# Optimization experiments

Hardware: AMD Instinct MI355X
Metric: run time of the kernel (lower is better)

## Reference

```python
import jax, jax.numpy as jnp
import numpy as np

N = 100_000      # nodes
E = 1_600_000    # edges
F_IN = 4         # num_features
H = 128          # hidden_channels
C = 5            # num_classes
G = 256          # graphs in batch


def setup_inputs() -> dict:
    key = jax.random.key(0)
    ks = jax.random.split(key, 14)
    x = jax.random.normal(ks[0], (N, F_IN), dtype=jnp.float32)
    edge_index = jax.random.randint(ks[1], (2, E), 0, N, dtype=jnp.int64)
    batch = jnp.sort(jax.random.randint(ks[2], (N,), 0, G, dtype=jnp.int64))
    def lin(k, fan_in, fan_out):
        kw, kb = jax.random.split(k)
        s = 1.0 / np.sqrt(fan_in)
        W = jax.random.uniform(kw, (fan_in, fan_out), jnp.float32, -s, s)
        b = jax.random.uniform(kb, (fan_out,), jnp.float32, -s, s)
        return W, b
    W1, b1 = lin(ks[3], F_IN, H)
    W2, b2 = lin(ks[4], H, H)
    W3, b3 = lin(ks[5], H, H)
    W4, b4 = lin(ks[6], H, H)
    Wl, bl = lin(ks[7], H, C)
    return {"x": x, "edge_index": edge_index, "batch": batch,
            "W1": W1, "b1": b1, "W2": W2, "b2": b2,
            "W3": W3, "b3": b3, "W4": W4, "b4": b4,
            "Wl": Wl, "bl": bl}


def reference(x, edge_index, batch, W1, b1, W2, b2, W3, b3, W4, b4, Wl, bl):
    n = x.shape[0]
    loop = jnp.arange(n, dtype=edge_index.dtype)
    src = jnp.concatenate([edge_index[0], loop])  # [E+N], with self-loops
    dst = jnp.concatenate([edge_index[1], loop])
    # symmetric normalization on A + I (PyG GCNConv default)
    deg = jax.ops.segment_sum(jnp.ones_like(dst, dtype=x.dtype), dst, num_segments=n)
    dinv = deg ** -0.5  # deg >= 1 thanks to self-loops
    coef = dinv[src] * dinv[dst]  # per-edge norm [E+N]

    def conv(h, W, b):
        h = h @ W                               # [N, H]
        msg = h[src] * coef[:, None]            # gather + scale [E+N, H]
        return jax.ops.segment_sum(msg, dst, num_segments=n) + b

    h = jax.nn.relu(conv(x, W1, b1))
    h = jax.nn.relu(conv(h, W2, b2))
    h = jax.nn.relu(conv(h, W3, b3))
    h = jax.nn.relu(conv(h, W4, b4))

    # global_mean_pool over graph ids
    counts = jax.ops.segment_sum(jnp.ones((n,), h.dtype), batch, num_segments=G)
    pooled = jax.ops.segment_sum(h, batch, num_segments=G)
    pooled = pooled / jnp.maximum(counts, 1.0)[:, None]  # [G, H]

    return jax.nn.sigmoid(pooled @ Wl + bl)  # [G, C]
```

## Files before the change

kernel.cpp:

```cpp
#include <hip/hip_runtime.h>
#include <hip/hip_fp8.h>
#include <math.h>

#define N_NODES 100000
#define N_EDGES 1600000
#define F_IN    4
#define HID     128
#define N_CLS   5
#define N_GRAPH 256
#define POOL_SEG 8

#define BSHIFT   9
#define BSIZE    512
#define NBUK     196
#define NCHUNK   200
#define CHUNK    8000

typedef _Float16 f16;
typedef _Float16 f16x2 __attribute__((ext_vector_type(2)));
typedef _Float16 f16x8 __attribute__((ext_vector_type(8)));
typedef float f32x4 __attribute__((ext_vector_type(4)));

__device__ __forceinline__ float rec_coef(unsigned r) {
    return (float)__builtin_bit_cast(_Float16, (unsigned short)(r & 0x7FFFu));
}

__device__ __forceinline__ f16x2 rec_coef2(unsigned r) {
    unsigned c = r & 0x7FFFu;
    return __builtin_bit_cast(f16x2, (c << 16) | c);
}

__device__ __forceinline__ float2 fp8x2_to_f32x2(unsigned short raw) {
    __hip_fp8x2_e4m3 t;
    t.__x = raw;
    return static_cast<float2>(t);
}

#if __has_builtin(__builtin_amdgcn_cvt_pk_f16_fp8)
__device__ __forceinline__ f16x2 cvt_h2(unsigned v) {
    auto t = __builtin_amdgcn_cvt_pk_f16_fp8((short)v);
    return __builtin_bit_cast(f16x2, t);
}
#else
__device__ __forceinline__ f16x2 cvt_h2(unsigned v) {
    float2 f = fp8x2_to_f32x2((unsigned short)v);
    auto t = __builtin_amdgcn_cvt_pkrtz(f.x, f.y);
    return __builtin_bit_cast(f16x2, t);
}
#endif

__device__ __forceinline__ void fma8h(f16x2 c2, uint2 v, f16x2* acc) {
    acc[0] += c2 * cvt_h2(v.x);
    acc[1] += c2 * cvt_h2(v.x >> 16);
    acc[2] += c2 * cvt_h2(v.y);
    acc[3] += c2 * cvt_h2(v.y >> 16);
}

__device__ __forceinline__ f16x2 shfl_xor_h2(f16x2 a, int m) {
    return __builtin_bit_cast(f16x2, __shfl_xor(__builtin_bit_cast(int, a), m, 64));
}

__global__ __launch_bounds__(256) void k_bc(const int* __restrict__ dst, int* __restrict__ C) {
    __shared__ int cnt[NBUK];
    int t = threadIdx.x;
    if (t < NBUK) cnt[t] = 0;
    __syncthreads();
    int base = blockIdx.x * CHUNK;
#pragma unroll
    for (int it = 0; it < 32; ++it) {
        int idx = it * 256 + t;
        if (idx < CHUNK) atomicAdd(&cnt[dst[base + idx] >> BSHIFT], 1);
    }
    __syncthreads();
    if (t < NBUK) C[blockIdx.x * NBUK + t] = cnt[t];
}

__global__ __launch_bounds__(256) void k_bscan(const int* __restrict__ C, int* __restrict__ Off,
                                               int* __restrict__ bbase) {
    __shared__ int s[256];
    int b = threadIdx.x;
    int tot = 0;
    if (b < NBUK) {
        for (int c = 0; c < NCHUNK; ++c) {
            Off[c * NBUK + b] = tot;
            tot += C[c * NBUK + b];
        }
    }
    s[b] = (b < NBUK) ? tot : 0;
    __syncthreads();
    for (int off = 1; off < 256; off <<= 1) {
        int v = (b >= off) ? s[b - off] : 0;
        __syncthreads();
        s[b] += v;
        __syncthreads();
    }
    if (b < NBUK) bbase[b] = s[b] - tot;
    if (b == 0) bbase[NBUK] = N_EDGES;
}

__global__ __launch_bounds__(256) void k_scatter(const int* __restrict__ src, const int* __restrict__ dst,
                                                 const int* __restrict__ Off, const int* __restrict__ bbase,
                                                 unsigned* __restrict__ bkt) {
    __shared__ int cur[NBUK];
    int t = threadIdx.x;
    if (t < NBUK) cur[t] = bbase[t] + Off[blockIdx.x * NBUK + t];
    __syncthreads();
    int base = blockIdx.x * CHUNK;
#pragma unroll
    for (int it = 0; it < 32; ++it) {
        int idx = it * 256 + t;
        if (idx < CHUNK) {
            int s = src[base + idx], d = dst[base + idx];
            int b = d >> BSHIFT;
            int p = atomicAdd(&cur[b], 1);
            bkt[p] = ((unsigned)s << BSHIFT) | (unsigned)(d & (BSIZE - 1));
        }
    }
}

__global__ __launch_bounds__(256) void k_hist2(const unsigned* __restrict__ bkt,
                                               const int* __restrict__ bbase,
                                               int* __restrict__ deg, float* __restrict__ dinv,
                                               int* __restrict__ padTot) {
    __shared__ int hist[BSIZE];
    __shared__ int tot;
    int t = threadIdx.x, b = blockIdx.x;
    hist[t] = 0; hist[t + 256] = 0;
    if (t == 0) tot = 0;
    __syncthreads();
    int s0 = bbase[b], s1 = bbase[b + 1];
    for (int e = s0 + t; e < s1; e += 256) atomicAdd(&hist[bkt[e] & (BSIZE - 1)], 1);
    __syncthreads();
    int loc = 0;
#pragma unroll
    for (int h = 0; h < 2; ++h) {
        int l = t + h * 256;
        int node = b * BSIZE + l;
        int d = hist[l];
        if (node < N_NODES) {
            deg[node] = d;
            dinv[node] = rsqrtf((float)d + 1.0f);
        }
        loc += (d + 15) >> 4;
    }
    atomicAdd(&tot, loc);
    __syncthreads();
    if (t == 0) padTot[b] = tot << 4;
}

__global__ __launch_bounds__(256) void k_pscan(const int* __restrict__ padTot, int* __restrict__ padBase,
                                               int* __restrict__ rowptrP) {
    __shared__ int s[256];
    int b = threadIdx.x;
    int v = (b < NBUK) ? padTot[b] : 0;
    s[b] = v;
    __syncthreads();
    for (int off = 1; off < 256; off <<= 1) {
        int u = (b >= off) ? s[b - off] : 0;
        __syncthreads();
        s[b] += u;
        __syncthreads();
    }
    if (b < NBUK) padBase[b] = s[b] - v;
    if (b == 0) {
        padBase[NBUK] = s[NBUK - 1];
        rowptrP[N_NODES] = s[NBUK - 1];
    }
}

__global__ __launch_bounds__(256) void k_local2(const unsigned* __restrict__ bkt,
                                                const int* __restrict__ bbase,
                                                const int* __restrict__ deg,
                                                const float* __restrict__ dinv,
                                                const int* __restrict__ padBase,
                                                int* __restrict__ rowptrP,
                                                unsigned* __restrict__ edges) {
    __shared__ int sc[BSIZE];
    __shared__ int cur[BSIZE];
    __shared__ int st[BSIZE];
    __shared__ float dv[BSIZE];
    int t = threadIdx.x, b = blockIdx.x;
    int base = padBase[b];
    int n0 = b * BSIZE + t, n1 = n0 + 256;
    int d0 = (n0 < N_NODES) ? deg[n0] : 0;
    int d1 = (n1 < N_NODES) ? deg[n1] : 0;
    int p0 = ((d0 + 15) >> 4) << 4;
    int p1 = ((d1 + 15) >> 4) << 4;
    sc[t] = p0; sc[t + 256] = p1;
    dv[t] = (n0 < N_NODES) ? dinv[n0] : 0.f;
    dv[t + 256] = (n1 < N_NODES) ? dinv[n1] : 0.f;
    __syncthreads();
    for (int off = 1; off < BSIZE; off <<= 1) {
        int i0 = t, i1 = t + 256;
        int v0 = (i0 >= off) ? sc[i0 - off] : 0;
        int v1 = (i1 >= off) ? sc[i1 - off] : 0;
        __syncthreads();
        sc[i0] += v0; sc[i1] += v1;
        __syncthreads();
    }
    int off0 = base + sc[t] - p0;
    int off1 = base + sc[t + 256] - p1;
    if (n0 < N_NODES) rowptrP[n0] = off0;
    if (n1 < N_NODES) rowptrP[n1] = off1;
    cur[t] = off0; cur[t + 256] = off1;
    st[t]  = off0; st[t + 256]  = off1;
    int padT = sc[BSIZE - 1];
    for (int i = base + t; i < base + padT; i += 256) edges[i] = 0;
    __syncthreads();
    int s0 = bbase[b], s1 = bbase[b + 1];
    for (int e = s0 + t; e < s1; e += 256) {
        unsigned r = bkt[e];
        int dl = (int)(r & (BSIZE - 1));
        int s = (int)(r >> BSHIFT);
        int p = atomicAdd(&cur[dl], 1);
        int rs = st[dl];
        int sl = p - rs;
        int phys = rs + (sl & ~15) + (((sl & 3) << 2) | ((sl >> 2) & 3));
        float c = dv[dl] * dinv[s];
        unsigned short cb = __builtin_bit_cast(unsigned short, (f16)c);
        edges[phys] = ((unsigned)s << 15) | (unsigned)(cb & 0x7FFFu);
    }
}

__global__ __launch_bounds__(256) void k_aggx1(const float4* __restrict__ x,
                                               const int* __restrict__ rowptrP,
                                               const unsigned* __restrict__ edges,
                                               const float* __restrict__ dinv,
                                               const float* __restrict__ W1, const float* __restrict__ b1,
                                               unsigned* __restrict__ hA) {
    __shared__ float4 sxa[16];
    __shared__ float sW[4 * HID];
    __shared__ float sb[HID];
    int t = threadIdx.x;
    sW[t] = W1[t];
    sW[t + 256] = W1[t + 256];
    if (t < HID) sb[t] = b1[t];
    int grp = t >> 4;
    int l = t & 15;
    int node = blockIdx.x * 16 + grp;
    int beg = rowptrP[node], end = rowptrP[node + 1];
    float ax = 0.f, ay = 0.f, az = 0.f, aw = 0.f;
    for (int e = beg + l; e < end; e += 16) {
        unsigned r = edges[e];
        float c = rec_coef(r);
        float4 v = x[r >> 15];
        ax = fmaf(c, v.x, ax); ay = fmaf(c, v.y, ay);
        az = fmaf(c, v.z, az); aw = fmaf(c, v.w, aw);
    }
#pragma unroll
    for (int off = 1; off < 16; off <<= 1) {
        ax += __shfl_xor(ax, off, 64);
        ay += __shfl_xor(ay, off, 64);
        az += __shfl_xor(az, off, 64);
        aw += __shfl_xor(aw, off, 64);
    }
    if (l == 0) {
        float di = dinv[node];
        float c0 = di * di;
        float4 xv = x[node];
        sxa[grp] = make_float4(fmaf(c0, xv.x, ax), fmaf(c0, xv.y, ay),
                               fmaf(c0, xv.z, az), fmaf(c0, xv.w, aw));
    }
    __syncthreads();

    int node0 = blockIdx.x * 16;
#pragma unroll
    for (int it = 0; it < 2; ++it) {
        int id = it * 256 + t;
        int n = id >> 5;
        int g = id & 31;
        float4 a = sxa[n];
        float c[4];
#pragma unroll
        for (int j = 0; j < 4; ++j) {
            int col = g * 4 + j;
            float v = sb[col];
            v = fmaf(a.x, sW[col],           v);
            v = fmaf(a.y, sW[HID + col],     v);
            v = fmaf(a.z, sW[2 * HID + col], v);
            v = fmaf(a.w, sW[3 * HID + col], v);
            c[j] = fmaxf(v, 0.0f);
        }
        unsigned lo = __hip_fp8x2_e4m3(make_float2(c[0], c[1])).__x;
        unsigned hi = __hip_fp8x2_e4m3(make_float2(c[2], c[3])).__x;
        hA[(node0 + n) * 32 + g] = lo | (hi << 16);
    }
}

template <bool FP8OUT>
__global__ __launch_bounds__(1024, 8) void k_aggemm8(const unsigned* __restrict__ h8,
                                                     const int* __restrict__ rowptrP,
                                                     const unsigned* __restrict__ edges,
                                                     const float* __restrict__ dinv,
                                                     const f16* __restrict__ Wp,
                                                     const float* __restrict__ bias,
                                                     void* __restrict__ outv) {
    __shared__ f16 S[32 * HID];
    int wave = threadIdx.x >> 6;
    int lane = threadIdx.x & 63;
    int half = lane >> 5;
    int g    = (lane >> 4) & 1;
    int l    = lane & 15;
    int node0 = blockIdx.x * 32;
    int row   = wave * 2 + half;
    int node  = node0 + row;
    int beg = rowptrP[node];
    int end = rowptrP[node + 1];
    const char* hp = (const char*)h8 + l * 8;

    f16x2 acc[4];
    acc[0] = (f16x2){0, 0}; acc[1] = (f16x2){0, 0};
    acc[2] = (f16x2){0, 0}; acc[3] = (f16x2){0, 0};
    {
        float di = dinv[node];
        f16 c0 = (g == 0) ? (f16)(di * di) : (f16)0.f;
        f16x2 c02; c02.x = c0; c02.y = c0;
        uint2 v = *(const uint2*)(hp + ((size_t)node << 7));
        fma8h(c02, v, acc);
    }

    for (int e = beg; e < end; e += 8) {
        uint4 R = *(const uint4*)(edges + e + g * 4);
        unsigned rr[4] = {R.x, R.y, R.z, R.w};
#pragma unroll
        for (int i = 0; i < 4; ++i) {
            unsigned rec = rr[i];
            uint2 v = *(const uint2*)(hp + ((rec >> 8) & 0xFFFFFF80u));
            fma8h(rec_coef2(rec), v, acc);
        }
    }

#pragma unroll
    for (int j = 0; j < 4; ++j) acc[j] += shfl_xor_h2(acc[j], 16);

    if ((lane & 16) == 0) {
        f16x8 o;
        o[0] = acc[0][0]; o[1] = acc[0][1]; o[2] = acc[1][0]; o[3] = acc[1][1];
        o[4] = acc[2][0]; o[5] = acc[2][1]; o[6] = acc[3][0]; o[7] = acc[3][1];
        int dw = (l * 4) ^ ((row & 7) << 2);
        *(f16x8*)&S[row * HID + dw * 2] = o;
    }
    __syncthreads();

    {
        int t  = wave >> 1;
        int rt = wave & 1;
        int m = lane & 15;
        int q = lane >> 4;
        f32x4 c4 = (f32x4){0.f, 0.f, 0.f, 0.f};
#pragma unroll
        for (int ks = 0; ks < 4; ++ks) {
            int dw = (ks * 16 + q * 4) ^ ((m & 7) << 2);
            f16x8 a = *(const f16x8*)&S[(rt * 16 + m) * HID + dw * 2];
            f16x8 b = *(const f16x8*)(Wp + ((size_t)(t * 4 + ks) * 64 + lane) * 8);
            c4 = __builtin_amdgcn_mfma_f32_16x16x32_f16(a, b, c4, 0, 0, 0);
        }
        float bb = bias[t * 16 + m];
#pragma unroll
        for (int r = 0; r < 4; ++r) {
            float val = fmaxf(c4[r] + bb, 0.0f);
            int orow = node0 + rt * 16 + q * 4 + r;
            if constexpr (FP8OUT) {
                ((__hip_fp8_e4m3*)outv)[(size_t)orow * HID + t * 16 + m] = __hip_fp8_e4m3(val);
            } else {
                ((f16*)outv)[(size_t)orow * HID + t * 16 + m] = (f16)val;
            }
        }
    }
}

__global__ __launch_bounds__(256) void k_packW3(const float* __restrict__ W2, const float* __restrict__ W3,
                                                const float* __restrict__ W4, f16* __restrict__ Wp) {
    int idx = blockIdx.x * 256 + threadIdx.x;
    int which = idx >> 14;
    int r = idx & 16383;
    const float* W = (which == 0) ? W2 : (which == 1) ? W3 : W4;
    int j  = r & 7;
    int L  = (r >> 3) & 63;
    int ks = (r >> 9) & 3;
    int ct = r >> 11;
    int k = ks * 32 + (L >> 4) * 8 + j;
    int n = ct * 16 + (L & 15);
    Wp[idx] = (f16)W[k * HID + n];
}

__device__ __forceinline__ int lower_bound_batch(const int* __restrict__ batch, int val) {
    int lo = 0, hi = N_NODES;
    while (lo < hi) { int m = (lo + hi) >> 1; if (batch[m] < val) lo = m + 1; else hi = m; }
    return lo;
}

__global__ __launch_bounds__(128) void k_pool1(const f16* __restrict__ h, const int* __restrict__ batch,
                                               float* __restrict__ partials) {
    int g = blockIdx.x / POOL_SEG;
    int s = blockIdx.x % POOL_SEG;
    int f = threadIdx.x;
    int beg = lower_bound_batch(batch, g);
    int end = lower_bound_batch(batch, g + 1);
    int len = end - beg;
    int sb = beg + (int)(((long long)len * s) / POOL_SEG);
    int se = beg + (int)(((long long)len * (s + 1)) / POOL_SEG);
    float acc = 0.0f;
    for (int i = sb; i < se; ++i) acc += (float)h[i * HID + f];
    partials[(size_t)blockIdx.x * HID + f] = acc;
}

__global__ __launch_bounds__(128) void k_pool2h(const float* __restrict__ partials,
                                                const int* __restrict__ batch,
                                                const float* __restrict__ Wl, const float* __restrict__ bl,
                                                float* __restrict__ out) {
    __shared__ float sp[HID];
    int g = blockIdx.x;
    int f = threadIdx.x;
    float acc = 0.0f;
#pragma unroll
    for (int s = 0; s < POOL_SEG; ++s)
        acc += partials[(size_t)(g * POOL_SEG + s) * HID + f];
    int beg = lower_bound_batch(batch, g);
    int end = lower_bound_batch(batch, g + 1);
    sp[f] = acc / fmaxf((float)(end - beg), 1.0f);
    __syncthreads();
    if (f < N_CLS) {
        float v = bl[f];
        for (int k = 0; k < HID; ++k) v = fmaf(sp[k], Wl[k * N_CLS + f], v);
        out[g * N_CLS + f] = 1.0f / (1.0f + expf(-v));
    }
}

extern "C" void kernel_launch(void* const* d_in, const int* in_sizes, int n_in,
                              void* d_out, int out_size, void* d_ws, size_t ws_size,
                              hipStream_t stream) {
    const float* x     = (const float*)d_in[0];
    const int*   ei    = (const int*)d_in[1];
    const int*   batch = (const int*)d_in[2];
    const float* W1 = (const float*)d_in[3];  const float* b1 = (const float*)d_in[4];
    const float* W2 = (const float*)d_in[5];  const float* b2 = (const float*)d_in[6];
    const float* W3 = (const float*)d_in[7];  const float* b3 = (const float*)d_in[8];
    const float* W4 = (const float*)d_in[9];  const float* b4 = (const float*)d_in[10];
    const float* Wl = (const float*)d_in[11]; const float* bl = (const float*)d_in[12];
    float* out = (float*)d_out;

    const size_t EPAD = (size_t)N_EDGES + (size_t)N_NODES * 16;

    char* p = (char*)d_ws;
    auto alloc = [&](size_t bytes) { char* r = p; p += (bytes + 255) & ~(size_t)255; return (void*)r; };
    int*      C       = (int*)     alloc((size_t)NCHUNK * NBUK * 4);
    int*      Off     = (int*)     alloc((size_t)NCHUNK * NBUK * 4);
    int*      bbase   = (int*)     alloc((size_t)(NBUK + 1) * 4);
    int*      padTot  = (int*)     alloc((size_t)NBUK * 4);
    int*      padBase = (int*)     alloc((size_t)(NBUK + 1) * 4);
    unsigned* bkt     = (unsigned*)alloc((size_t)N_EDGES * 4);
    int*      deg     = (int*)     alloc((size_t)N_NODES * 4);
    int*      rowptrP = (int*)     alloc((size_t)(N_NODES + 1) * 4);
    float*    dinv    = (float*)   alloc((size_t)N_NODES * 4);
    unsigned* edges   = (unsigned*)alloc(EPAD * 4);
    unsigned* hA      = (unsigned*)alloc((size_t)N_NODES * HID);
    unsigned* hC      = (unsigned*)alloc((size_t)N_NODES * HID);
    f16*      h4      = (f16*)     alloc((size_t)N_NODES * HID * 2);
    float*    parts   = (float*)   alloc((size_t)N_GRAPH * POOL_SEG * HID * 4);
    f16*      Wp      = (f16*)     alloc((size_t)3 * HID * HID * 2);
    f16*      Wp2 = Wp;
    f16*      Wp3 = Wp + HID * HID;
    f16*      Wp4 = Wp + 2 * HID * HID;

    const int* srcv = ei;
    const int* dstv = ei + N_EDGES;

    k_bc     <<<NCHUNK, 256, 0, stream>>>(dstv, C);
    k_bscan  <<<1, 256, 0, stream>>>(C, Off, bbase);
    k_scatter<<<NCHUNK, 256, 0, stream>>>(srcv, dstv, Off, bbase, bkt);
    k_hist2  <<<NBUK, 256, 0, stream>>>(bkt, bbase, deg, dinv, padTot);
    k_pscan  <<<1, 256, 0, stream>>>(padTot, padBase, rowptrP);
    k_local2 <<<NBUK, 256, 0, stream>>>(bkt, bbase, deg, dinv, padBase, rowptrP, edges);

    k_packW3<<<192, 256, 0, stream>>>(W2, W3, W4, Wp);

    k_aggx1<<<N_NODES / 16, 256, 0, stream>>>((const float4*)x, rowptrP, edges, dinv, W1, b1, hA);

    const int fgrid = N_NODES / 32;
    k_aggemm8<true ><<<fgrid, 1024, 0, stream>>>(hA, rowptrP, edges, dinv, Wp2, b2, hC);
    k_aggemm8<true ><<<fgrid, 1024, 0, stream>>>(hC, rowptrP, edges, dinv, Wp3, b3, hA);
    k_aggemm8<false><<<fgrid, 1024, 0, stream>>>(hA, rowptrP, edges, dinv, Wp4, b4, h4);

    k_pool1 <<<N_GRAPH * POOL_SEG, 128, 0, stream>>>(h4, batch, parts);
    k_pool2h<<<N_GRAPH, 128, 0, stream>>>(parts, batch, Wl, bl, out);
}
```

Measured before the change: 347.0 us.

## Pad CSR rows to 8, prefetch edge gathers, shrink aggregation blocks

Row padding in the CSR edge list drops from multiples of 16 to multiples of 8, with the interleaved physical layout adjusted to match. This cuts the padded zero-edges processed per node. The aggregation loop is software-pipelined so the next edge records and feature gathers are issued before the current FMAs, hiding gather latency. Blocks shrink from 32 nodes/1024 threads to 16 nodes/512 threads, each wave handling one MFMA column tile; this trades more blocks and more reloads of Wp for better load balance.

```diff
diff --git a/kernel.cpp b/kernel.cpp
--- a/kernel.cpp
+++ b/kernel.cpp
@@ -141,11 +141,11 @@
             deg[node] = d;
             dinv[node] = rsqrtf((float)d + 1.0f);
         }
-        loc += (d + 15) >> 4;
+        loc += (d + 7) >> 3;
     }
     atomicAdd(&tot, loc);
     __syncthreads();
-    if (t == 0) padTot[b] = tot << 4;
+    if (t == 0) padTot[b] = tot << 3;
 }
 
 __global__ __launch_bounds__(256) void k_pscan(const int* __restrict__ padTot, int* __restrict__ padBase,
@@ -184,8 +184,8 @@
     int n0 = b * BSIZE + t, n1 = n0 + 256;
     int d0 = (n0 < N_NODES) ? deg[n0] : 0;
     int d1 = (n1 < N_NODES) ? deg[n1] : 0;
-    int p0 = ((d0 + 15) >> 4) << 4;
-    int p1 = ((d1 + 15) >> 4) << 4;
+    int p0 = ((d0 + 7) >> 3) << 3;
+    int p1 = ((d1 + 7) >> 3) << 3;
     sc[t] = p0; sc[t + 256] = p1;
     dv[t] = (n0 < N_NODES) ? dinv[n0] : 0.f;
     dv[t + 256] = (n1 < N_NODES) ? dinv[n1] : 0.f;
@@ -215,7 +215,7 @@
         int p = atomicAdd(&cur[dl], 1);
         int rs = st[dl];
         int sl = p - rs;
-        int phys = rs + (sl & ~15) + (((sl & 3) << 2) | ((sl >> 2) & 3));
+        int phys = rs + (sl & ~7) + (((sl & 1) << 2) | ((sl >> 1) & 3));
         float c = dv[dl] * dinv[s];
         unsigned short cb = __builtin_bit_cast(unsigned short, (f16)c);
         edges[phys] = ((unsigned)s << 15) | (unsigned)(cb & 0x7FFFu);
@@ -288,20 +288,20 @@
 }
 
 template <bool FP8OUT>
-__global__ __launch_bounds__(1024, 8) void k_aggemm8(const unsigned* __restrict__ h8,
-                                                     const int* __restrict__ rowptrP,
-                                                     const unsigned* __restrict__ edges,
-                                                     const float* __restrict__ dinv,
-                                                     const f16* __restrict__ Wp,
-                                                     const float* __restrict__ bias,
-                                                     void* __restrict__ outv) {
-    __shared__ f16 S[32 * HID];
+__global__ __launch_bounds__(512, 8) void k_aggemm8(const unsigned* __restrict__ h8,
+                                                    const int* __restrict__ rowptrP,
+                                                    const unsigned* __restrict__ edges,
+                                                    const float* __restrict__ dinv,
+                                                    const f16* __restrict__ Wp,
+                                                    const float* __restrict__ bias,
+                                                    void* __restrict__ outv) {
+    __shared__ f16 S[16 * HID];
     int wave = threadIdx.x >> 6;
     int lane = threadIdx.x & 63;
     int half = lane >> 5;
     int g    = (lane >> 4) & 1;
     int l    = lane & 15;
-    int node0 = blockIdx.x * 32;
+    int node0 = blockIdx.x * 16;
     int row   = wave * 2 + half;
     int node  = node0 + row;
     int beg = rowptrP[node];
@@ -319,14 +319,29 @@
         fma8h(c02, v, acc);
     }
 
-    for (int e = beg; e < end; e += 8) {
-        uint4 R = *(const uint4*)(edges + e + g * 4);
-        unsigned rr[4] = {R.x, R.y, R.z, R.w};
-#pragma unroll
-        for (int i = 0; i < 4; ++i) {
-            unsigned rec = rr[i];
-            uint2 v = *(const uint2*)(hp + ((rec >> 8) & 0xFFFFFF80u));
-            fma8h(rec_coef2(rec), v, acc);
+    if (beg < end) {
+        uint4 R = *(const uint4*)(edges + beg + g * 4);
+        uint2 V0 = *(const uint2*)(hp + ((R.x >> 8) & 0xFFFFFF80u));
+        uint2 V1 = *(const uint2*)(hp + ((R.y >> 8) & 0xFFFFFF80u));
+        uint2 V2 = *(const uint2*)(hp + ((R.z >> 8) & 0xFFFFFF80u));
+        uint2 V3 = *(const uint2*)(hp + ((R.w >> 8) & 0xFFFFFF80u));
+        int e = beg;
+        while (true) {
+            int en = e + 8;
+            bool more = en < end;
+            uint4 Rc = R;
+            uint2 W0 = V0, W1 = V1, W2 = V2, W3 = V3;
+            if (more) R = *(const uint4*)(edges + en + g * 4);
+            fma8h(rec_coef2(Rc.x), W0, acc);
+            fma8h(rec_coef2(Rc.y), W1, acc);
+            fma8h(rec_coef2(Rc.z), W2, acc);
+            fma8h(rec_coef2(Rc.w), W3, acc);
+            if (!more) break;
+            V0 = *(const uint2*)(hp + ((R.x >> 8) & 0xFFFFFF80u));
+            V1 = *(const uint2*)(hp + ((R.y >> 8) & 0xFFFFFF80u));
+            V2 = *(const uint2*)(hp + ((R.z >> 8) & 0xFFFFFF80u));
+            V3 = *(const uint2*)(hp + ((R.w >> 8) & 0xFFFFFF80u));
+            e = en;
         }
     }
 
@@ -343,15 +358,14 @@
     __syncthreads();
 
     {
-        int t  = wave >> 1;
-        int rt = wave & 1;
+        int t = wave;
         int m = lane & 15;
         int q = lane >> 4;
         f32x4 c4 = (f32x4){0.f, 0.f, 0.f, 0.f};
 #pragma unroll
         for (int ks = 0; ks < 4; ++ks) {
             int dw = (ks * 16 + q * 4) ^ ((m & 7) << 2);
-            f16x8 a = *(const f16x8*)&S[(rt * 16 + m) * HID + dw * 2];
+            f16x8 a = *(const f16x8*)&S[m * HID + dw * 2];
             f16x8 b = *(const f16x8*)(Wp + ((size_t)(t * 4 + ks) * 64 + lane) * 8);
             c4 = __builtin_amdgcn_mfma_f32_16x16x32_f16(a, b, c4, 0, 0, 0);
         }
@@ -359,7 +373,7 @@
 #pragma unroll
         for (int r = 0; r < 4; ++r) {
             float val = fmaxf(c4[r] + bb, 0.0f);
-            int orow = node0 + rt * 16 + q * 4 + r;
+            int orow = node0 + q * 4 + r;
             if constexpr (FP8OUT) {
                 ((__hip_fp8_e4m3*)outv)[(size_t)orow * HID + t * 16 + m] = __hip_fp8_e4m3(val);
             } else {
@@ -477,10 +491,10 @@
 
     k_aggx1<<<N_NODES / 16, 256, 0, stream>>>((const float4*)x, rowptrP, edges, dinv, W1, b1, hA);
 
-    const int fgrid = N_NODES / 32;
-    k_aggemm8<true ><<<fgrid, 1024, 0, stream>>>(hA, rowptrP, edges, dinv, Wp2, b2, hC);
-    k_aggemm8<true ><<<fgrid, 1024, 0, stream>>>(hC, rowptrP, edges, dinv, Wp3, b3, hA);
-    k_aggemm8<false><<<fgrid, 1024, 0, stream>>>(hA, rowptrP, edges, dinv, Wp4, b4, h4);
+    const int fgrid = N_NODES / 16;
+    k_aggemm8<true ><<<fgrid, 512, 0, stream>>>(hA, rowptrP, edges, dinv, Wp2, b2, hC);
+    k_aggemm8<true ><<<fgrid, 512, 0, stream>>>(hC, rowptrP, edges, dinv, Wp3, b3, hA);
+    k_aggemm8<false><<<fgrid, 512, 0, stream>>>(hA, rowptrP, edges, dinv, Wp4, b4, h4);
 
     k_pool1 <<<N_GRAPH * POOL_SEG, 128, 0, stream>>>(h4, batch, parts);
     k_pool2h<<<N_GRAPH, 128, 0, stream>>>(parts, batch, Wl, bl, out);
```

Measured after the change: 319.3 us. -8.0%, faster.
